# Kernel tuning notes

Hardware: AMD Instinct MI355X
Metric: run time of the kernel (lower is better)

## Reference

```python
import jax, jax.numpy as jnp
import numpy as np

GROUPS = 32
EPS = 1e-5
NUM_HEADS = 8


def group_norm(x, gamma, beta):
    B, C, H, W = x.shape
    xg = x.reshape(B, GROUPS, C // GROUPS, H, W)
    mean = xg.mean(axis=(2, 3, 4), keepdims=True)
    var = xg.var(axis=(2, 3, 4), keepdims=True)
    xg = (xg - mean) * jax.lax.rsqrt(var + EPS)
    x = xg.reshape(B, C, H, W)
    return x * gamma[None, :, None, None] + beta[None, :, None, None]


def setup_inputs() -> dict:
    key = jax.random.key(0)
    k1, k2, k3 = jax.random.split(key, 3)
    C = 512
    x = jax.random.normal(k1, (16, C, 32, 32), dtype=jnp.float32)
    gn_gamma = jnp.ones((C,), dtype=jnp.float32)
    gn_beta = jnp.zeros((C,), dtype=jnp.float32)
    w_qkv = jax.random.normal(k2, (3 * C, C), dtype=jnp.float32) * 0.02
    b_qkv = jnp.zeros((3 * C,), dtype=jnp.float32)
    w_proj = jax.random.normal(k3, (C, C), dtype=jnp.float32) * 0.02
    b_proj = jnp.zeros((C,), dtype=jnp.float32)
    return {"x": x, "gn_gamma": gn_gamma, "gn_beta": gn_beta,
            "w_qkv": w_qkv, "b_qkv": b_qkv, "w_proj": w_proj, "b_proj": b_proj}


def reference(x, gn_gamma, gn_beta, w_qkv, b_qkv, w_proj, b_proj):
    B, C, H, W = x.shape
    nh = NUM_HEADS
    hd = C // nh
    h = group_norm(x, gn_gamma, gn_beta)
    # 1x1 conv == channel matmul: [B,3C,H,W]
    qkv = jnp.einsum('bchw,oc->bohw', h, w_qkv) + b_qkv[None, :, None, None]
    qkv = qkv.reshape(B, 3, nh, hd, H * W)
    q, k, v = qkv[:, 0], qkv[:, 1], qkv[:, 2]  # [B, nh, hd, HW]
    scale = hd ** -0.5
    # attn[b,n,i,j] = sum_d q[b,n,d,i] * k[b,n,d,j]
    attn = jax.nn.softmax(jnp.einsum('bndi,bndj->bnij', q, k) * scale, axis=-1)
    # h[b,n,d,i] = sum_j v[b,n,d,j] * attn[b,n,i,j]
    h = jnp.einsum('bndj,bnij->bndi', v, attn).reshape(B, C, H, W)
    out = jnp.einsum('bchw,oc->bohw', h, w_proj) + b_proj[None, :, None, None]
    return x + out
```

## Files before the change

### kernel.cpp

```cpp
#include <hip/hip_runtime.h>

typedef __bf16 bf16;
typedef __bf16 bf16x4 __attribute__((ext_vector_type(4)));
typedef __bf16 bf16x8 __attribute__((ext_vector_type(8)));
typedef float  f32x4  __attribute__((ext_vector_type(4)));

#define MFMA(a,b,c) __builtin_amdgcn_mfma_f32_16x16x32_bf16((a),(b),(c),0,0,0)

__device__ __forceinline__ void gll16(const void* g, void* l) {
  __builtin_amdgcn_global_load_lds((const __attribute__((address_space(1))) unsigned int*)g,
                                   (__attribute__((address_space(3))) unsigned int*)l, 16, 0, 0);
}

static constexpr int Cc = 512;
static constexpr int Ss = 1024;
#define QSCALE 0.18033688011112042f

__global__ __launch_bounds__(256) void k_wconv(const float* __restrict__ wq, const float* __restrict__ wp,
                                               bf16* __restrict__ wqb, bf16* __restrict__ wpb) {
  const int i = blockIdx.x * 256 + threadIdx.x;
  if (i * 4 < 786432) {
    float4 v = ((const float4*)wq)[i];
    bf16x4 o = { (bf16)v.x, (bf16)v.y, (bf16)v.z, (bf16)v.w };
    ((bf16x4*)wqb)[i] = o;
  } else {
    const int j = i - 786432 / 4;
    float4 v = ((const float4*)wp)[j];
    bf16x4 o = { (bf16)v.x, (bf16)v.y, (bf16)v.z, (bf16)v.w };
    ((bf16x4*)wpb)[j] = o;
  }
}

__global__ __launch_bounds__(256, 2) void k_gnorm(const float* __restrict__ x,
                                                  const float* __restrict__ gamma,
                                                  const float* __restrict__ beta,
                                                  bf16* __restrict__ ht) {
  const int g = blockIdx.x;
  const int b = blockIdx.y;
  const float* base = x + ((size_t)b * Cc + g * 16) * Ss;
  const int tid = threadIdx.x;

  f32x4 xr[16];
  float s = 0.f, sq = 0.f;
  #pragma unroll
  for (int k = 0; k < 16; ++k) {
    xr[k] = ((const f32x4*)base)[k * 256 + tid];
    s  += xr[k][0] + xr[k][1] + xr[k][2] + xr[k][3];
    sq += xr[k][0] * xr[k][0] + xr[k][1] * xr[k][1] + xr[k][2] * xr[k][2] + xr[k][3] * xr[k][3];
  }
  #pragma unroll
  for (int m = 1; m < 64; m <<= 1) { s += __shfl_xor(s, m); sq += __shfl_xor(sq, m); }
  __shared__ float red[8];
  if ((tid & 63) == 0) { red[tid >> 6] = s; red[4 + (tid >> 6)] = sq; }
  __syncthreads();
  const float stot = red[0] + red[1] + red[2] + red[3];
  const float sqt  = red[4] + red[5] + red[6] + red[7];
  const float mean = stot * (1.f / 16384.f);
  const float var  = sqt * (1.f / 16384.f) - mean * mean;
  const float rstd = rsqrtf(var + 1e-5f);

  float ga[16], bb[16];
  #pragma unroll
  for (int k = 0; k < 16; ++k) {
    ga[k] = gamma[g * 16 + k] * rstd;
    bb[k] = beta[g * 16 + k] - mean * ga[k];
  }

  bf16* dst0 = ht + ((size_t)b * Ss + tid * 4) * Cc + g * 16;
  #pragma unroll
  for (int j = 0; j < 4; ++j) {
    bf16x8 o0, o1;
    #pragma unroll
    for (int k = 0; k < 8; ++k)  o0[k] = (bf16)(xr[k][j] * ga[k] + bb[k]);
    #pragma unroll
    for (int k = 0; k < 8; ++k)  o1[k] = (bf16)(xr[8 + k][j] * ga[8 + k] + bb[8 + k]);
    bf16* d = dst0 + (size_t)j * Cc;
    *(bf16x8*)d = o0;
    *(bf16x8*)(d + 8) = o1;
  }
}

template<int MODE>
__global__ __launch_bounds__(256) void k_gemm(const bf16* __restrict__ Aw,
                                              const bf16* __restrict__ Bt,
                                              const float* __restrict__ bias,
                                              bf16* __restrict__ qo, bf16* __restrict__ ko,
                                              bf16* __restrict__ vo,
                                              const float* __restrict__ xres,
                                              float* __restrict__ out) {
  const int nt = blockIdx.x, mt = blockIdx.y, b = blockIdx.z;
  const int M0 = mt * 128, N0 = nt * 128;
  __shared__ __align__(16) bf16 lA[128 * 64];
  __shared__ __align__(16) bf16 lB[128 * 64];
  const int tid = threadIdx.x;
  const int l = tid & 63, w = tid >> 6;
  const int wm = w >> 1, wn = w & 1;
  const int l15 = l & 15, gq = l >> 4;
  const bf16* Bb = Bt + (size_t)b * Ss * Cc;
  const int rowS = tid >> 3;
  const int cb = (tid & 7) * 16;

  f32x4 acc[4][4];
  #pragma unroll
  for (int i = 0; i < 4; ++i)
    #pragma unroll
    for (int j = 0; j < 4; ++j) acc[i][j] = f32x4{0.f, 0.f, 0.f, 0.f};

  for (int kt = 0; kt < 8; ++kt) {
    #pragma unroll
    for (int p = 0; p < 4; ++p) {
      const int r = p * 32 + rowS;
      gll16((const char*)Aw + ((size_t)(M0 + r) * 512 + kt * 64) * 2 + cb,
            (char*)lA + p * 4096 + tid * 16);
    }
    #pragma unroll
    for (int p = 0; p < 4; ++p) {
      const int r = p * 32 + rowS;
      gll16((const char*)Bb + ((size_t)(N0 + r) * 512 + kt * 64) * 2 + cb,
            (char*)lB + p * 4096 + tid * 16);
    }
    __syncthreads();
    #pragma unroll
    for (int kk = 0; kk < 2; ++kk) {
      bf16x8 af[4], bfr[4];
      #pragma unroll
      for (int mf = 0; mf < 4; ++mf)
        af[mf] = *(const bf16x8*)((const char*)lA + (wm * 64 + mf * 16 + l15) * 128 + kk * 64 + gq * 16);
      #pragma unroll
      for (int nf = 0; nf < 4; ++nf)
        bfr[nf] = *(const bf16x8*)((const char*)lB + (wn * 64 + nf * 16 + l15) * 128 + kk * 64 + gq * 16);
      #pragma unroll
      for (int mf = 0; mf < 4; ++mf)
        #pragma unroll
        for (int nf = 0; nf < 4; ++nf)
          acc[mf][nf] = MFMA(af[mf], bfr[nf], acc[mf][nf]);
    }
    __syncthreads();
  }

  #pragma unroll
  for (int mf = 0; mf < 4; ++mf) {
    const int ofr = M0 + wm * 64 + mf * 16;
    float bi[4];
    #pragma unroll
    for (int r = 0; r < 4; ++r) bi[r] = bias[ofr + gq * 4 + r];
    #pragma unroll
    for (int nf = 0; nf < 4; ++nf) {
      const int sI = N0 + wn * 64 + nf * 16 + l15;
      f32x4 v = acc[mf][nf];
      if (MODE == 0) {
        const int which = ofr >> 9;
        const int nh = (ofr >> 6) & 7;
        const int dbase = (ofr & 63) + gq * 4;
        const size_t bh = (size_t)b * 8 + nh;
        if (which == 2) {
          #pragma unroll
          for (int r = 0; r < 4; ++r)
            vo[(bh * 64 + dbase + r) * 1024 + sI] = (bf16)(v[r] + bi[r]);
        } else {
          const float qs = which ? 1.f : QSCALE;
          bf16x4 pk = { (bf16)((v[0] + bi[0]) * qs), (bf16)((v[1] + bi[1]) * qs),
                        (bf16)((v[2] + bi[2]) * qs), (bf16)((v[3] + bi[3]) * qs) };
          bf16* dst = (which ? ko : qo) + (bh * 1024 + sI) * 64 + dbase;
          *(bf16x4*)dst = pk;
        }
      } else {
        #pragma unroll
        for (int r = 0; r < 4; ++r) {
          const size_t idx = ((size_t)b * 512 + ofr + gq * 4 + r) * 1024 + sI;
          out[idx] = xres[idx] + bi[r] + v[r];
        }
      }
    }
  }
}

__global__ __launch_bounds__(512, 4) void k_attn(const bf16* __restrict__ qT,
                                                 const bf16* __restrict__ kT,
                                                 const bf16* __restrict__ vv,
                                                 bf16* __restrict__ ao) {
  const int it = blockIdx.x, nh = blockIdx.y, b = blockIdx.z;
  const size_t bh = (size_t)b * 8 + nh;
  const char* kh = (const char*)(kT + bh * 65536);
  const char* vh = (const char*)(vv + bh * 65536);
  __shared__ __align__(16) char smem[65536];
  const int tid = threadIdx.x;
  const int w = tid >> 6, l = tid & 63;
  const int l15 = l & 15, g = l >> 4;
  char* lpw = smem + 49152 + w * 2048;
  const int swq = (l15 & 7) << 4;

  const int rowS = tid >> 3;
  const int cb = (tid & 7) * 16;
  const int sw = cb ^ ((rowS & 7) << 4);
  const char* ksrc = kh + rowS * 128 + sw;
  const char* vsrc = vh + rowS * 2048 + sw;
  char* lkdst = smem + tid * 16;
  char* lvdst = smem + 24576 + tid * 16;

  const bf16* qrow = qT + bh * 65536 + (size_t)(it * 128 + w * 16 + l15) * 64;
  const bf16x8 aq0 = *(const bf16x8*)(qrow + g * 8);
  const bf16x8 aq1 = *(const bf16x8*)(qrow + 32 + g * 8);

  int offR[2][4];
  #pragma unroll
  for (int kk = 0; kk < 2; ++kk)
    #pragma unroll
    for (int nf = 0; nf < 4; ++nf) {
      const int r = nf * 16 + l15;
      offR[kk][nf] = r * 128 + ((kk * 64 + g * 16) ^ ((r & 7) << 4));
    }
  int offPw[4];
  #pragma unroll
  for (int nf = 0; nf < 4; ++nf) offPw[nf] = l15 * 128 + ((nf * 32 + g * 8) ^ swq);
  const int offPr0 = l15 * 128 + ((g * 16) ^ swq);
  const int offPr1 = l15 * 128 + ((64 + g * 16) ^ swq);

  gll16(ksrc, lkdst);
  gll16(vsrc, lvdst);
  gll16(ksrc + 8192, lkdst + 8192);
  gll16(vsrc + 128, lvdst + 8192);

  const bf16 one1 = (bf16)1.0f;
  const bf16x8 vone = { one1, one1, one1, one1, one1, one1, one1, one1 };

  f32x4 oacc[4];
  #pragma unroll
  for (int df = 0; df < 4; ++df) oacc[df] = f32x4{0.f, 0.f, 0.f, 0.f};
  f32x4 oext = f32x4{0.f, 0.f, 0.f, 0.f};

  int scur = 0;
  for (int t = 0; t < 16; ++t) {
    if (t < 15) asm volatile("s_waitcnt vmcnt(2)" ::: "memory");
    else        asm volatile("s_waitcnt vmcnt(0)" ::: "memory");
    __builtin_amdgcn_s_barrier();
    __builtin_amdgcn_sched_barrier(0);
    if (t <= 13) {
      const int sn = (scur == 0) ? 2 : scur - 1;
      gll16(ksrc + (t + 2) * 8192, lkdst + sn * 8192);
      gll16(vsrc + (t + 2) * 128, lvdst + sn * 8192);
    }
    const char* lkc = smem + scur * 8192;
    const char* lvc = smem + 24576 + scur * 8192;

    f32x4 sf[4];
    #pragma unroll
    for (int nf = 0; nf < 4; ++nf) sf[nf] = f32x4{0.f, 0.f, 0.f, 0.f};
    __builtin_amdgcn_s_setprio(1);
    #pragma unroll
    for (int kk = 0; kk < 2; ++kk) {
      const bf16x8 aq = kk ? aq1 : aq0;
      #pragma unroll
      for (int nf = 0; nf < 4; ++nf) {
        bf16x8 bk = *(const bf16x8*)(lkc + offR[kk][nf]);
        sf[nf] = MFMA(bk, aq, sf[nf]);
      }
    }
    __builtin_amdgcn_s_setprio(0);
    #pragma unroll
    for (int nf = 0; nf < 4; ++nf) {
      const float p0 = exp2f(sf[nf][0]), p1 = exp2f(sf[nf][1]),
                  p2 = exp2f(sf[nf][2]), p3 = exp2f(sf[nf][3]);
      bf16x4 pk = { (bf16)p0, (bf16)p1, (bf16)p2, (bf16)p3 };
      *(bf16x4*)(lpw + offPw[nf]) = pk;
    }
    const bf16x8 pa0 = *(const bf16x8*)(lpw + offPr0);
    const bf16x8 pa1 = *(const bf16x8*)(lpw + offPr1);
    __builtin_amdgcn_s_setprio(1);
    oext = MFMA(pa0, vone, oext);
    oext = MFMA(pa1, vone, oext);
    #pragma unroll
    for (int jj = 0; jj < 2; ++jj) {
      const bf16x8 pa = jj ? pa1 : pa0;
      #pragma unroll
      for (int df = 0; df < 4; ++df) {
        bf16x8 bv = *(const bf16x8*)(lvc + offR[jj][df]);
        oacc[df] = MFMA(pa, bv, oacc[df]);
      }
    }
    __builtin_amdgcn_s_setprio(0);
    scur = (scur == 2) ? 0 : scur + 1;
  }

  float rinv[4];
  #pragma unroll
  for (int r = 0; r < 4; ++r) rinv[r] = 1.f / oext[r];
  #pragma unroll
  for (int df = 0; df < 4; ++df) {
    #pragma unroll
    for (int r = 0; r < 4; ++r) {
      const int i = it * 128 + w * 16 + g * 4 + r;
      ao[((size_t)b * 1024 + i) * 512 + nh * 64 + df * 16 + l15] = (bf16)(oacc[df][r] * rinv[r]);
    }
  }
}

extern "C" void kernel_launch(void* const* d_in, const int* in_sizes, int n_in,
                              void* d_out, int out_size, void* d_ws, size_t ws_size,
                              hipStream_t stream) {
  (void)in_sizes; (void)n_in; (void)out_size; (void)ws_size;
  const float* x   = (const float*)d_in[0];
  const float* gam = (const float*)d_in[1];
  const float* bet = (const float*)d_in[2];
  const float* wq  = (const float*)d_in[3];
  const float* bq  = (const float*)d_in[4];
  const float* wp  = (const float*)d_in[5];
  const float* bp  = (const float*)d_in[6];
  float* out = (float*)d_out;

  bf16* ws  = (bf16*)d_ws;
  bf16* ht  = ws;
  bf16* qT  = ws + 8388608;
  bf16* kT  = ws + 16777216;
  bf16* vv  = ws + 25165824;
  bf16* wqb = ws + 33554432;
  bf16* wpb = ws + 34340864;

  k_wconv<<<1024, 256, 0, stream>>>(wq, wp, wqb, wpb);
  k_gnorm<<<dim3(32, 16), 256, 0, stream>>>(x, gam, bet, ht);
  k_gemm<0><<<dim3(8, 12, 16), 256, 0, stream>>>(wqb, ht, bq, qT, kT, vv, nullptr, nullptr);
  k_attn<<<dim3(8, 8, 16), 512, 0, stream>>>(qT, kT, vv, ht);
  k_gemm<1><<<dim3(8, 4, 16), 256, 0, stream>>>(wpb, ht, bp, nullptr, nullptr, nullptr, x, out);
}
```

Measured before the change: 151.2 us.

## Rewrite attention kernel with 32x32 MFMA and register-resident P via permlane swap

The attention kernel moves from 16x16x32 to 32x32x16 bf16 MFMA tiles, with each wave covering 32 query rows and each block 256 queries (grid halved). The softmax probabilities no longer round-trip through LDS: they are packed in registers and rearranged with v_permlane32_swap to form the PV operand, and the row sums are accumulated in scalar registers instead of an extra MFMA against a ones vector. The pipeline shrinks from a triple-buffered LDS ring to double buffering with a __syncthreads per iteration, and exp2 uses the hardware builtin. Fewer blocks and lower occupancy (launch bounds 3) trade parallelism for more work per wave and less LDS traffic.

Measured after the change: 136.2 us. 1.11x faster.

```diff
diff --git a/kernel.cpp b/kernel.cpp
--- a/kernel.cpp
+++ b/kernel.cpp
@@ -1,15 +1,34 @@
 #include <hip/hip_runtime.h>
 
 typedef __bf16 bf16;
+typedef __bf16 bf16x2 __attribute__((ext_vector_type(2)));
 typedef __bf16 bf16x4 __attribute__((ext_vector_type(4)));
 typedef __bf16 bf16x8 __attribute__((ext_vector_type(8)));
 typedef float  f32x4  __attribute__((ext_vector_type(4)));
-
-#define MFMA(a,b,c) __builtin_amdgcn_mfma_f32_16x16x32_bf16((a),(b),(c),0,0,0)
+typedef float  f32x16 __attribute__((ext_vector_type(16)));
+typedef unsigned int u32x4 __attribute__((ext_vector_type(4)));
+
+#define MFMA(a,b,c)   __builtin_amdgcn_mfma_f32_16x16x32_bf16((a),(b),(c),0,0,0)
+#define MFMA32(a,b,c) __builtin_amdgcn_mfma_f32_32x32x16_bf16((a),(b),(c),0,0,0)
+
+#if __has_builtin(__builtin_amdgcn_exp2f)
+#define EXP2(x) __builtin_amdgcn_exp2f(x)
+#else
+#define EXP2(x) exp2f(x)
+#endif
 
 __device__ __forceinline__ void gll16(const void* g, void* l) {
   __builtin_amdgcn_global_load_lds((const __attribute__((address_space(1))) unsigned int*)g,
                                    (__attribute__((address_space(3))) unsigned int*)l, 16, 0, 0);
+}
+
+__device__ __forceinline__ unsigned pk2(float a, float b) {
+  bf16x2 t = { (bf16)a, (bf16)b };
+  return __builtin_bit_cast(unsigned, t);
+}
+
+__device__ __forceinline__ void pl32swap(unsigned &x, unsigned &y) {
+  asm("v_permlane32_swap_b32 %0, %1" : "+v"(x), "+v"(y));
 }
 
 static constexpr int Cc = 512;
@@ -175,7 +194,7 @@
   }
 }
 
-__global__ __launch_bounds__(512, 4) void k_attn(const bf16* __restrict__ qT,
+__global__ __launch_bounds__(512, 3) void k_attn(const bf16* __restrict__ qT,
                                                  const bf16* __restrict__ kT,
                                                  const bf16* __restrict__ vv,
                                                  bf16* __restrict__ ao) {
@@ -183,114 +202,109 @@
   const size_t bh = (size_t)b * 8 + nh;
   const char* kh = (const char*)(kT + bh * 65536);
   const char* vh = (const char*)(vv + bh * 65536);
-  __shared__ __align__(16) char smem[65536];
+  __shared__ __align__(16) char smem[32768];
   const int tid = threadIdx.x;
   const int w = tid >> 6, l = tid & 63;
-  const int l15 = l & 15, g = l >> 4;
-  char* lpw = smem + 49152 + w * 2048;
-  const int swq = (l15 & 7) << 4;
-
-  const int rowS = tid >> 3;
-  const int cb = (tid & 7) * 16;
-  const int sw = cb ^ ((rowS & 7) << 4);
-  const char* ksrc = kh + rowS * 128 + sw;
-  const char* vsrc = vh + rowS * 2048 + sw;
+  const int l31 = l & 31, h = l >> 5;
+
+  const int ct = tid >> 6, c3 = ct & 3, c2 = ct >> 2;
+  const char* ksrc = kh + (size_t)(c2 * 32 + l31) * 128 + c3 * 32 + h * 16;
+  const char* vsrc = vh + (size_t)(c2 * 32 + l31) * 2048 + c3 * 32 + h * 16;
   char* lkdst = smem + tid * 16;
-  char* lvdst = smem + 24576 + tid * 16;
-
-  const bf16* qrow = qT + bh * 65536 + (size_t)(it * 128 + w * 16 + l15) * 64;
-  const bf16x8 aq0 = *(const bf16x8*)(qrow + g * 8);
-  const bf16x8 aq1 = *(const bf16x8*)(qrow + 32 + g * 8);
-
-  int offR[2][4];
-  #pragma unroll
-  for (int kk = 0; kk < 2; ++kk)
-    #pragma unroll
-    for (int nf = 0; nf < 4; ++nf) {
-      const int r = nf * 16 + l15;
-      offR[kk][nf] = r * 128 + ((kk * 64 + g * 16) ^ ((r & 7) << 4));
-    }
-  int offPw[4];
-  #pragma unroll
-  for (int nf = 0; nf < 4; ++nf) offPw[nf] = l15 * 128 + ((nf * 32 + g * 8) ^ swq);
-  const int offPr0 = l15 * 128 + ((g * 16) ^ swq);
-  const int offPr1 = l15 * 128 + ((64 + g * 16) ^ swq);
+  char* lvdst = smem + 16384 + tid * 16;
+
+  const bf16* qrow = qT + bh * 65536 + (size_t)(it * 256 + w * 32 + l31) * 64;
+  bf16x8 qf[4];
+  #pragma unroll
+  for (int kq = 0; kq < 4; ++kq) qf[kq] = *(const bf16x8*)(qrow + kq * 16 + h * 8);
 
   gll16(ksrc, lkdst);
   gll16(vsrc, lvdst);
-  gll16(ksrc + 8192, lkdst + 8192);
-  gll16(vsrc + 128, lvdst + 8192);
-
-  const bf16 one1 = (bf16)1.0f;
-  const bf16x8 vone = { one1, one1, one1, one1, one1, one1, one1, one1 };
-
-  f32x4 oacc[4];
-  #pragma unroll
-  for (int df = 0; df < 4; ++df) oacc[df] = f32x4{0.f, 0.f, 0.f, 0.f};
-  f32x4 oext = f32x4{0.f, 0.f, 0.f, 0.f};
-
-  int scur = 0;
+
+  f32x16 oacc[2];
+  #pragma unroll
+  for (int dt = 0; dt < 2; ++dt)
+    #pragma unroll
+    for (int r = 0; r < 16; ++r) oacc[dt][r] = 0.f;
+  float lacc0 = 0.f, lacc1 = 0.f;
+
+  __syncthreads();
+
+  int cur = 0;
   for (int t = 0; t < 16; ++t) {
-    if (t < 15) asm volatile("s_waitcnt vmcnt(2)" ::: "memory");
-    else        asm volatile("s_waitcnt vmcnt(0)" ::: "memory");
-    __builtin_amdgcn_s_barrier();
-    __builtin_amdgcn_sched_barrier(0);
-    if (t <= 13) {
-      const int sn = (scur == 0) ? 2 : scur - 1;
-      gll16(ksrc + (t + 2) * 8192, lkdst + sn * 8192);
-      gll16(vsrc + (t + 2) * 128, lvdst + sn * 8192);
-    }
-    const char* lkc = smem + scur * 8192;
-    const char* lvc = smem + 24576 + scur * 8192;
-
-    f32x4 sf[4];
-    #pragma unroll
-    for (int nf = 0; nf < 4; ++nf) sf[nf] = f32x4{0.f, 0.f, 0.f, 0.f};
+    if (t < 15) {
+      gll16(ksrc + (size_t)(t + 1) * 8192, lkdst + (cur ^ 1) * 8192);
+      gll16(vsrc + (size_t)(t + 1) * 128,  lvdst + (cur ^ 1) * 8192);
+    }
+    const char* lkc = smem + cur * 8192;
+    const char* lvc = smem + 16384 + cur * 8192;
+
+    f32x16 sf[2];
+    #pragma unroll
+    for (int r = 0; r < 16; ++r) { sf[0][r] = 0.f; sf[1][r] = 0.f; }
     __builtin_amdgcn_s_setprio(1);
     #pragma unroll
-    for (int kk = 0; kk < 2; ++kk) {
-      const bf16x8 aq = kk ? aq1 : aq0;
-      #pragma unroll
-      for (int nf = 0; nf < 4; ++nf) {
-        bf16x8 bk = *(const bf16x8*)(lkc + offR[kk][nf]);
-        sf[nf] = MFMA(bk, aq, sf[nf]);
+    for (int kq = 0; kq < 4; ++kq) {
+      bf16x8 a0 = *(const bf16x8*)(lkc + kq * 1024 + l * 16);
+      bf16x8 a1 = *(const bf16x8*)(lkc + (4 + kq) * 1024 + l * 16);
+      sf[0] = MFMA32(a0, qf[kq], sf[0]);
+      sf[1] = MFMA32(a1, qf[kq], sf[1]);
+    }
+    __builtin_amdgcn_s_setprio(0);
+
+    unsigned pw[2][4][2];
+    #pragma unroll
+    for (int jt = 0; jt < 2; ++jt) {
+      #pragma unroll
+      for (int Qi = 0; Qi < 4; ++Qi) {
+        const float p0 = EXP2(sf[jt][Qi * 4 + 0]);
+        const float p1 = EXP2(sf[jt][Qi * 4 + 1]);
+        const float p2 = EXP2(sf[jt][Qi * 4 + 2]);
+        const float p3 = EXP2(sf[jt][Qi * 4 + 3]);
+        lacc0 += p0 + p1; lacc1 += p2 + p3;
+        pw[jt][Qi][0] = pk2(p0, p1);
+        pw[jt][Qi][1] = pk2(p2, p3);
       }
     }
+
+    bf16x8 pb[4];
+    #pragma unroll
+    for (int s = 0; s < 4; ++s) {
+      const int jt = s >> 1, sq = s & 1;
+      unsigned x0 = pw[jt][2 * sq][0], y0 = pw[jt][2 * sq + 1][0];
+      unsigned x1 = pw[jt][2 * sq][1], y1 = pw[jt][2 * sq + 1][1];
+      pl32swap(x0, y0);
+      pl32swap(x1, y1);
+      u32x4 wv = { x0, x1, y0, y1 };
+      pb[s] = __builtin_bit_cast(bf16x8, wv);
+    }
+
+    __builtin_amdgcn_s_setprio(1);
+    #pragma unroll
+    for (int dt = 0; dt < 2; ++dt) {
+      #pragma unroll
+      for (int s = 0; s < 4; ++s) {
+        bf16x8 av = *(const bf16x8*)(lvc + (dt * 4 + s) * 1024 + l * 16);
+        oacc[dt] = MFMA32(av, pb[s], oacc[dt]);
+      }
+    }
     __builtin_amdgcn_s_setprio(0);
-    #pragma unroll
-    for (int nf = 0; nf < 4; ++nf) {
-      const float p0 = exp2f(sf[nf][0]), p1 = exp2f(sf[nf][1]),
-                  p2 = exp2f(sf[nf][2]), p3 = exp2f(sf[nf][3]);
-      bf16x4 pk = { (bf16)p0, (bf16)p1, (bf16)p2, (bf16)p3 };
-      *(bf16x4*)(lpw + offPw[nf]) = pk;
-    }
-    const bf16x8 pa0 = *(const bf16x8*)(lpw + offPr0);
-    const bf16x8 pa1 = *(const bf16x8*)(lpw + offPr1);
-    __builtin_amdgcn_s_setprio(1);
-    oext = MFMA(pa0, vone, oext);
-    oext = MFMA(pa1, vone, oext);
-    #pragma unroll
-    for (int jj = 0; jj < 2; ++jj) {
-      const bf16x8 pa = jj ? pa1 : pa0;
-      #pragma unroll
-      for (int df = 0; df < 4; ++df) {
-        bf16x8 bv = *(const bf16x8*)(lvc + offR[jj][df]);
-        oacc[df] = MFMA(pa, bv, oacc[df]);
-      }
-    }
-    __builtin_amdgcn_s_setprio(0);
-    scur = (scur == 2) ? 0 : scur + 1;
-  }
-
-  float rinv[4];
-  #pragma unroll
-  for (int r = 0; r < 4; ++r) rinv[r] = 1.f / oext[r];
-  #pragma unroll
-  for (int df = 0; df < 4; ++df) {
-    #pragma unroll
-    for (int r = 0; r < 4; ++r) {
-      const int i = it * 128 + w * 16 + g * 4 + r;
-      ao[((size_t)b * 1024 + i) * 512 + nh * 64 + df * 16 + l15] = (bf16)(oacc[df][r] * rinv[r]);
+    __syncthreads();
+    cur ^= 1;
+  }
+
+  float ls = lacc0 + lacc1;
+  ls += __shfl_xor(ls, 32);
+  const float rinv = 1.f / ls;
+
+  bf16* aor = ao + ((size_t)b * 1024 + it * 256 + w * 32 + l31) * 512 + nh * 64;
+  #pragma unroll
+  for (int dt = 0; dt < 2; ++dt) {
+    #pragma unroll
+    for (int Qi = 0; Qi < 4; ++Qi) {
+      bf16x4 o = { (bf16)(oacc[dt][Qi * 4 + 0] * rinv), (bf16)(oacc[dt][Qi * 4 + 1] * rinv),
+                   (bf16)(oacc[dt][Qi * 4 + 2] * rinv), (bf16)(oacc[dt][Qi * 4 + 3] * rinv) };
+      *(bf16x4*)(aor + dt * 32 + Qi * 8 + h * 4) = o;
     }
   }
 }
@@ -319,6 +333,6 @@
   k_wconv<<<1024, 256, 0, stream>>>(wq, wp, wqb, wpb);
   k_gnorm<<<dim3(32, 16), 256, 0, stream>>>(x, gam, bet, ht);
   k_gemm<0><<<dim3(8, 12, 16), 256, 0, stream>>>(wqb, ht, bq, qT, kT, vv, nullptr, nullptr);
-  k_attn<<<dim3(8, 8, 16), 512, 0, stream>>>(qT, kT, vv, ht);
+  k_attn<<<dim3(4, 8, 16), 512, 0, stream>>>(qT, kT, vv, ht);
   k_gemm<1><<<dim3(8, 4, 16), 256, 0, stream>>>(wpb, ht, bp, nullptr, nullptr, nullptr, x, out);
 }
```
